# Performance work log

Hardware: AMD Instinct MI355X
Metric: run time of the kernel (lower is better)

## Reference

```python
import jax, jax.numpy as jnp
import numpy as np

# FFM: 20 fields x 500 features each, k=16
NUM_FIELDS = 20
FIELD_SIZE = 500
TOTAL_FEATURES = NUM_FIELDS * FIELD_SIZE  # 10000
K = 16
BATCH = 4096


def setup_inputs() -> dict:
    key = jax.random.key(0)
    kx, kw, kv = jax.random.split(key, 3)
    x = jax.random.uniform(kx, (BATCH, TOTAL_FEATURES), dtype=jnp.float32)
    w = jax.random.normal(kw, (TOTAL_FEATURES, 1), dtype=jnp.float32)
    v = jax.random.normal(kv, (NUM_FIELDS, TOTAL_FEATURES, K), dtype=jnp.float32)
    return {"x": x, "w": w, "v": v}


def reference(x, w, v):
    B = x.shape[0]
    F, S, k = NUM_FIELDS, FIELD_SIZE, K
    # linear term: [B, 1]
    linear = x @ w
    # group features by field (fields are contiguous, equal-sized)
    xr = x.reshape(B, F, S)            # [b, field i, feat within field]
    vr = v.reshape(F, F, S, k)         # [field g (other), field i, feat, k]
    # E[b, g, i, :] = sum over features of field i of x * v[g]
    # i.e. field-i embedding specialized for interaction with field g
    E = jnp.einsum('bis,gisk->bgik', xr, vr)  # [B, F, F, K]
    # pairwise term: sum_{i<j} <E[b, j, i], E[b, i, j]>
    T = jnp.einsum('bjik,bijk->bij', E, E)    # [B, F, F]
    mask = jnp.triu(jnp.ones((F, F), dtype=bool), 1)
    pair = jnp.sum(jnp.where(mask, T, 0.0), axis=(1, 2))[:, None]  # [B, 1]
    return linear + pair
```

## Files before the change

kernel.cpp:

```cpp
#include <hip/hip_runtime.h>
#include <stdint.h>


#define NF 20
#define FS 500
#define TFEAT 10000
#define KD 16
#define NCOL 336
#define NFRG 21
#define KP 512
#define NB 4096
#define ROWE (NF * NCOL)

typedef __bf16 bf16x8 __attribute__((ext_vector_type(8)));
typedef __bf16 bf16x2 __attribute__((ext_vector_type(2)));
typedef float  f32x4  __attribute__((ext_vector_type(4)));
typedef unsigned int u32x4 __attribute__((ext_vector_type(4)));

typedef __attribute__((address_space(1))) const void* as1cv;
typedef __attribute__((address_space(3))) void* as3v;

__device__ inline void gload_lds16(const void* g, void* l) {
  __builtin_amdgcn_global_load_lds((as1cv)g, (as3v)l, 16, 0, 0);
}

__global__ __launch_bounds__(256) void prep_vt(const float* __restrict__ v,
                                               const float* __restrict__ w,
                                               __bf16* __restrict__ VtS) {
  const int i = blockIdx.x / NFRG;
  const int q = blockIdx.x % NFRG;
  const int tdx = threadIdx.x;
  __shared__ float lv[FS * 17];
  if (q < NF) {
    const int k = tdx & 15, sb = tdx >> 4;
    const float* vb = v + ((size_t)q * TFEAT + (size_t)i * FS) * KD;
    for (int it = 0; it < 32; ++it) {
      int s = it * 16 + sb;
      if (s < FS) lv[s * 17 + k] = vb[(size_t)s * KD + k];
    }
    __syncthreads();
  }
  const float* wf = w + (size_t)i * FS;
  __bf16* base = VtS + ((size_t)i * 16 * NFRG + q) * 512;
  for (int it = 0; it < 4; ++it) {
    int p = it * 256 + tdx;
    int t = p >> 6, l = p & 63;
    int r = l >> 2;
    int kk = t * 32 + (((l & 3) ^ ((l >> 3) & 3)) << 3);
    bf16x8 h;
#pragma unroll
    for (int e = 0; e < 8; ++e) {
      int s = kk + e;
      float val = 0.f;
      if (s < FS) {
        if (q < NF) val = lv[s * 17 + r];
        else if (r == 0) val = wf[s];
      }
      h[e] = (__bf16)val;
    }
    *(bf16x8*)(base + (size_t)t * (NFRG * 512) + l * 8) = h;
  }
}

__global__ __launch_bounds__(256, 3) void k1_gemm(
    const float* __restrict__ x, const __bf16* __restrict__ VtS,
    __bf16* __restrict__ E2, int chunk_base, int tiles) {
  __shared__ __bf16 As[2][64][32];
  __shared__ __bf16 Bs[2][NCOL * 32];

  int bid = blockIdx.x;
  const int nwg = gridDim.x;
  if ((nwg & 7) == 0) {
    int cpx = nwg >> 3;
    bid = (bid & 7) * cpx + (bid >> 3);
  }
  const int i  = bid / tiles;
  const int tb = bid % tiles;
  const int tid = threadIdx.x;
  const int lane = tid & 63, wid = tid >> 6;
  const int b0 = chunk_base + tb * 64;

  const int arow = tid >> 2;
  const int ac8 = (tid & 3) * 8;
  const int apch = (tid & 3) ^ ((tid >> 3) & 3);
  const float* xrow = x + (size_t)(b0 + arow) * TFEAT + i * FS;
  const __bf16* VtSi = VtS + (size_t)i * 16 * NFRG * 512 + lane * 8;

  auto issueB = [&](int t, int buf) {
#pragma unroll
    for (int jj = 0; jj < 6; ++jj) {
      int q = wid + 4 * jj;
      if (q < NFRG)
        gload_lds16(VtSi + ((size_t)t * NFRG + q) * 512,
                    (void*)&Bs[buf][q * 512]);
    }
  };

  f32x4 a0A, a1A, a0B, a1B;
  auto aload = [&](int t, f32x4& r0, f32x4& r1) {
    int kk = t * 32 + ac8;
    int c0 = kk > 496 ? 496 : kk;
    int c1 = kk + 4 > 496 ? 496 : kk + 4;
    r0 = *(const f32x4*)(xrow + c0);
    r1 = *(const f32x4*)(xrow + c1);
  };
  auto astore = [&](int buf, const f32x4& r0, const f32x4& r1) {
    bf16x8 h;
    h[0] = (__bf16)r0[0]; h[1] = (__bf16)r0[1];
    h[2] = (__bf16)r0[2]; h[3] = (__bf16)r0[3];
    h[4] = (__bf16)r1[0]; h[5] = (__bf16)r1[1];
    h[6] = (__bf16)r1[2]; h[7] = (__bf16)r1[3];
    *(bf16x8*)(&As[buf][arow][apch * 8]) = h;
  };

  const int nfr = wid ? 5 : 6;
  const int Fbase = wid ? (1 + wid * 5) : 0;
  const int ar = lane & 15, akc = lane >> 4;

  f32x4 acc[4][6];
#pragma unroll
  for (int m = 0; m < 4; ++m)
#pragma unroll
    for (int nf = 0; nf < 6; ++nf) acc[m][nf] = (f32x4){0.f, 0.f, 0.f, 0.f};

  aload(0, a0A, a1A);
  astore(0, a0A, a1A);
  issueB(0, 0);
  aload(1, a0B, a1B);
  asm volatile("s_waitcnt vmcnt(2) lgkmcnt(0)" ::: "memory");
  __builtin_amdgcn_s_barrier();

  auto body = [&](int T, int curbuf, f32x4& la0, f32x4& la1,
                  f32x4& sa0, f32x4& sa1) {
    if (T < 15) issueB(T + 1, curbuf ^ 1);
    if (T < 14) aload(T + 2, la0, la1);
    __builtin_amdgcn_sched_barrier(0);

    bf16x8 bfr[6];
#pragma unroll
    for (int nf = 0; nf < 6; ++nf)
      if (nf < nfr) {
        int n_ = (Fbase + nf) * 16 + ar;
        int pc = akc ^ ((n_ >> 1) & 3);
        bfr[nf] = *(const bf16x8*)&Bs[curbuf][n_ * 32 + pc * 8];
      }
#pragma unroll
    for (int m = 0; m < 4; ++m) {
      int row = m * 16 + ar;
      int pch = akc ^ ((row >> 1) & 3);
      bf16x8 af = *(const bf16x8*)(&As[curbuf][row][pch * 8]);
#pragma unroll
      for (int nf = 0; nf < 6; ++nf)
        if (nf < nfr)
          acc[m][nf] = __builtin_amdgcn_mfma_f32_16x16x32_bf16(af, bfr[nf],
                                                               acc[m][nf], 0, 0, 0);
    }
    if (T < 15) {
      astore(curbuf ^ 1, sa0, sa1);
      if (T < 14)
        asm volatile("s_waitcnt vmcnt(2) lgkmcnt(0)" ::: "memory");
      else
        asm volatile("s_waitcnt vmcnt(0) lgkmcnt(0)" ::: "memory");
      __builtin_amdgcn_s_barrier();
    }
  };

  for (int tt = 0; tt < 16; tt += 2) {
    body(tt,     0, a0A, a1A, a0B, a1B);
    body(tt + 1, 1, a0B, a1B, a0A, a1A);
  }

  const int lr4 = akc * 4, lcol = lane & 15;
#pragma unroll
  for (int m = 0; m < 4; ++m)
#pragma unroll
    for (int nf = 0; nf < 6; ++nf)
      if (nf < nfr) {
        int n = (Fbase + nf) * 16 + lcol;
#pragma unroll
        for (int r = 0; r < 4; ++r) {
          int bl = tb * 64 + m * 16 + lr4 + r;
          E2[(size_t)bl * ROWE + i * NCOL + n] = (__bf16)acc[m][nf][r];
        }
      }
}

__global__ __launch_bounds__(256) void k2_pair(
    const __bf16* __restrict__ E2, float* __restrict__ out, int chunk_base) {
  __shared__ __align__(16) unsigned shw[4][3360];
  const int tid = threadIdx.x, lane = tid & 63, wid = tid >> 6;
  const int bl = blockIdx.x * 4 + wid;
  const unsigned* src = (const unsigned*)(E2 + (size_t)bl * ROWE);
  for (int it = 0; it < 14; ++it) {
    int idx = it * 64 + lane;
    if (idx < 840) {
      u32x4 val = *(const u32x4*)(src + (size_t)idx * 4);
      *(u32x4*)&shw[wid][idx * 4] = val;
    }
  }
  __syncthreads();
  const __bf16* sh = (const __bf16*)shw[wid];
  const int k = lane & 15, g = lane >> 4;
  float sum = 0.f;
  for (int i = g; i < NF; i += 4)
    for (int j = i + 1; j < NF; ++j)
      sum += (float)sh[i * NCOL + j * 16 + k] * (float)sh[j * NCOL + i * 16 + k];
  if (lane < NF) sum += (float)sh[lane * NCOL + 320];
#pragma unroll
  for (int off = 32; off; off >>= 1) sum += __shfl_xor(sum, off);
  if (lane == 0) out[chunk_base + bl] = sum;
}

extern "C" void kernel_launch(void* const* d_in, const int* in_sizes, int n_in,
                              void* d_out, int out_size, void* d_ws, size_t ws_size,
                              hipStream_t stream) {
  const float* x = (const float*)d_in[0];
  const float* w = (const float*)d_in[1];
  const float* v = (const float*)d_in[2];
  float* out = (float*)d_out;
  char* ws = (char*)d_ws;

  const size_t vt_bytes = (size_t)NF * 16 * NFRG * 512 * 2;
  __bf16* VtS = (__bf16*)ws;
  __bf16* E2 = (__bf16*)(ws + vt_bytes);

  size_t eavail = (ws_size > vt_bytes) ? ws_size - vt_bytes : 0;
  int Bc = NB;
  while (Bc > 64 && (size_t)Bc * ROWE * 2 > eavail) Bc >>= 1;

  prep_vt<<<NF * NFRG, 256, 0, stream>>>(v, w, VtS);
  for (int cb = 0; cb < NB; cb += Bc) {
    int tiles = Bc / 64;
    k1_gemm<<<NF * tiles, 256, 0, stream>>>(x, VtS, E2, cb, tiles);
    k2_pair<<<Bc / 4, 256, 0, stream>>>(E2, out, cb);
  }
}
```

Baseline: 76.76 us.

## Triple-buffer LDS tiles in GEMM to prefetch B two stages ahead

Result: slower. 79.99 us (+4.2%).

```diff
diff --git a/kernel.cpp b/kernel.cpp
--- a/kernel.cpp
+++ b/kernel.cpp
@@ -8,7 +8,6 @@
 #define KD 16
 #define NCOL 336
 #define NFRG 21
-#define KP 512
 #define NB 4096
 #define ROWE (NF * NCOL)
 
@@ -62,11 +61,11 @@
   }
 }
 
-__global__ __launch_bounds__(256, 3) void k1_gemm(
+__global__ __launch_bounds__(256, 2) void k1_gemm(
     const float* __restrict__ x, const __bf16* __restrict__ VtS,
     __bf16* __restrict__ E2, int chunk_base, int tiles) {
-  __shared__ __bf16 As[2][64][32];
-  __shared__ __bf16 Bs[2][NCOL * 32];
+  __shared__ __bf16 As[3][64][32];
+  __shared__ __bf16 Bs[3][NCOL * 32];
 
   int bid = blockIdx.x;
   const int nwg = gridDim.x;
@@ -86,31 +85,31 @@
   const float* xrow = x + (size_t)(b0 + arow) * TFEAT + i * FS;
   const __bf16* VtSi = VtS + (size_t)i * 16 * NFRG * 512 + lane * 8;
 
-  auto issueB = [&](int t, int buf) {
+  auto issueB = [&](int t, int slot) {
 #pragma unroll
     for (int jj = 0; jj < 6; ++jj) {
       int q = wid + 4 * jj;
       if (q < NFRG)
         gload_lds16(VtSi + ((size_t)t * NFRG + q) * 512,
-                    (void*)&Bs[buf][q * 512]);
-    }
-  };
-
-  f32x4 a0A, a1A, a0B, a1B;
-  auto aload = [&](int t, f32x4& r0, f32x4& r1) {
+                    (void*)&Bs[slot][q * 512]);
+    }
+  };
+
+  f32x4 aS0[2], aS1[2], aS2[2];
+  auto aload = [&](int t, f32x4* r) {
     int kk = t * 32 + ac8;
     int c0 = kk > 496 ? 496 : kk;
     int c1 = kk + 4 > 496 ? 496 : kk + 4;
-    r0 = *(const f32x4*)(xrow + c0);
-    r1 = *(const f32x4*)(xrow + c1);
-  };
-  auto astore = [&](int buf, const f32x4& r0, const f32x4& r1) {
+    r[0] = *(const f32x4*)(xrow + c0);
+    r[1] = *(const f32x4*)(xrow + c1);
+  };
+  auto astore = [&](int slot, const f32x4* r) {
     bf16x8 h;
-    h[0] = (__bf16)r0[0]; h[1] = (__bf16)r0[1];
-    h[2] = (__bf16)r0[2]; h[3] = (__bf16)r0[3];
-    h[4] = (__bf16)r1[0]; h[5] = (__bf16)r1[1];
-    h[6] = (__bf16)r1[2]; h[7] = (__bf16)r1[3];
-    *(bf16x8*)(&As[buf][arow][apch * 8]) = h;
+#pragma unroll
+    for (int e = 0; e < 4; ++e) {
+      h[e] = (__bf16)r[0][e]; h[4 + e] = (__bf16)r[1][e];
+    }
+    *(bf16x8*)(&As[slot][arow][apch * 8]) = h;
   };
 
   const int nfr = wid ? 5 : 6;
@@ -123,51 +122,58 @@
 #pragma unroll
     for (int nf = 0; nf < 6; ++nf) acc[m][nf] = (f32x4){0.f, 0.f, 0.f, 0.f};
 
-  aload(0, a0A, a1A);
-  astore(0, a0A, a1A);
-  issueB(0, 0);
-  aload(1, a0B, a1B);
-  asm volatile("s_waitcnt vmcnt(2) lgkmcnt(0)" ::: "memory");
-  __builtin_amdgcn_s_barrier();
-
-  auto body = [&](int T, int curbuf, f32x4& la0, f32x4& la1,
-                  f32x4& sa0, f32x4& sa1) {
-    if (T < 15) issueB(T + 1, curbuf ^ 1);
-    if (T < 14) aload(T + 2, la0, la1);
-    __builtin_amdgcn_sched_barrier(0);
-
+  auto compute = [&](int slot) {
     bf16x8 bfr[6];
 #pragma unroll
     for (int nf = 0; nf < 6; ++nf)
       if (nf < nfr) {
         int n_ = (Fbase + nf) * 16 + ar;
         int pc = akc ^ ((n_ >> 1) & 3);
-        bfr[nf] = *(const bf16x8*)&Bs[curbuf][n_ * 32 + pc * 8];
+        bfr[nf] = *(const bf16x8*)&Bs[slot][n_ * 32 + pc * 8];
       }
 #pragma unroll
     for (int m = 0; m < 4; ++m) {
       int row = m * 16 + ar;
       int pch = akc ^ ((row >> 1) & 3);
-      bf16x8 af = *(const bf16x8*)(&As[curbuf][row][pch * 8]);
+      bf16x8 af = *(const bf16x8*)(&As[slot][row][pch * 8]);
 #pragma unroll
       for (int nf = 0; nf < 6; ++nf)
         if (nf < nfr)
           acc[m][nf] = __builtin_amdgcn_mfma_f32_16x16x32_bf16(af, bfr[nf],
                                                                acc[m][nf], 0, 0, 0);
     }
-    if (T < 15) {
-      astore(curbuf ^ 1, sa0, sa1);
-      if (T < 14)
-        asm volatile("s_waitcnt vmcnt(2) lgkmcnt(0)" ::: "memory");
+  };
+
+  issueB(0, 0);
+  aload(0, aS0);
+  issueB(1, 1);
+  aload(1, aS1);
+  astore(0, aS0);
+  __builtin_amdgcn_sched_barrier(0);
+  asm volatile("s_waitcnt vmcnt(8) lgkmcnt(0)" ::: "memory");
+  __builtin_amdgcn_s_barrier();
+
+#pragma unroll
+  for (int t = 0; t < 16; ++t) {
+    compute(t % 3);
+    if (t < 15) {
+      __builtin_amdgcn_sched_barrier(0);
+      if (t < 14) issueB(t + 2, (t + 2) % 3);
+      {
+        const int s1 = (t + 1) % 3;
+        astore(s1, s1 == 0 ? aS0 : (s1 == 1 ? aS1 : aS2));
+      }
+      if (t < 14) {
+        const int s2 = (t + 2) % 3;
+        aload(t + 2, s2 == 0 ? aS0 : (s2 == 1 ? aS1 : aS2));
+      }
+      __builtin_amdgcn_sched_barrier(0);
+      if (t < 14)
+        asm volatile("s_waitcnt vmcnt(8) lgkmcnt(0)" ::: "memory");
       else
         asm volatile("s_waitcnt vmcnt(0) lgkmcnt(0)" ::: "memory");
       __builtin_amdgcn_s_barrier();
     }
-  };
-
-  for (int tt = 0; tt < 16; tt += 2) {
-    body(tt,     0, a0A, a1A, a0B, a1B);
-    body(tt + 1, 1, a0B, a1B, a0A, a1A);
   }
 
   const int lr4 = akc * 4, lcol = lane & 15;
```
